# Kernel tuning notes

Measured on AMD Instinct MI355X. Metric: run time of the kernel, lower is better.

## Reference

```python
import jax, jax.numpy as jnp
import numpy as np

B = 16
L = 3600
LATENT = 64
D_MODEL = 128
D_INNER = 256   # expand * d_model
D_STATE = 16
D_CONV = 4
DT_RANK = 8     # ceil(d_model / 16)


def setup_inputs() -> dict:
    key = jax.random.key(0)
    ks = jax.random.split(key, 10)

    def w(k, shape, fan_in):
        return jax.random.normal(k, shape, jnp.float32) / np.float32(np.sqrt(fan_in))

    return {
        "z_sequence": jax.random.normal(ks[0], (B, L, LATENT), jnp.float32),
        # embedding Linear(latent_dim -> mamba_dim)
        "emb_w": w(ks[1], (D_MODEL, LATENT), LATENT),
        "emb_b": jnp.zeros((D_MODEL,), jnp.float32),
        # Mamba in_proj (no bias): d_model -> 2*d_inner
        "in_proj_w": w(ks[2], (2 * D_INNER, D_MODEL), D_MODEL),
        # depthwise causal conv1d (d_inner groups, kernel d_conv) + bias
        "conv_w": w(ks[3], (D_INNER, 1, D_CONV), D_CONV),
        "conv_b": jnp.zeros((D_INNER,), jnp.float32),
        # x_proj (no bias): d_inner -> dt_rank + 2*d_state
        "x_proj_w": w(ks[4], (DT_RANK + 2 * D_STATE, D_INNER), D_INNER),
        # dt_proj: dt_rank -> d_inner, bias init so softplus(b) ~ 0.01
        "dt_proj_w": w(ks[5], (D_INNER, DT_RANK), DT_RANK),
        "dt_proj_b": jnp.full((D_INNER,), np.log(np.expm1(0.01)), jnp.float32),
        # S4D-real init: A = -[1..d_state] per channel
        "A_log": jnp.log(jnp.broadcast_to(
            jnp.arange(1, D_STATE + 1, dtype=jnp.float32), (D_INNER, D_STATE))),
        "D_skip": jnp.ones((D_INNER,), jnp.float32),
        # out_proj (no bias): d_inner -> d_model
        "out_proj_w": w(ks[6], (D_MODEL, D_INNER), D_INNER),
        # LayerNorm(d_model)
        "norm_w": jnp.ones((D_MODEL,), jnp.float32),
        "norm_b": jnp.zeros((D_MODEL,), jnp.float32),
        # classifier Linear(d_model -> 1)
        "cls_w": w(ks[7], (1, D_MODEL), D_MODEL),
        "cls_b": jnp.zeros((1,), jnp.float32),
    }


def _forward(z_sequence, emb_w, emb_b, in_proj_w, conv_w, conv_b, x_proj_w,
             dt_proj_w, dt_proj_b, A_log, D_skip, out_proj_w,
             norm_w, norm_b, cls_w, cls_b):
    silu = jax.nn.silu
    # embedding: (B,L,latent) -> (B,L,d_model)
    x_emb = z_sequence @ emb_w.T + emb_b
    # Mamba in_proj -> x, z  each (B,L,d_inner)
    xz = x_emb @ in_proj_w.T
    x, z = jnp.split(xz, 2, axis=-1)
    # causal depthwise conv over time
    x_ncl = x.transpose(0, 2, 1)  # (B, d_inner, L)
    x_conv = jax.lax.conv_general_dilated(
        x_ncl, conv_w, window_strides=(1,), padding=[(D_CONV - 1, 0)],
        feature_group_count=D_INNER, dimension_numbers=("NCH", "OIH", "NCH"))
    x = silu(x_conv.transpose(0, 2, 1) + conv_b)  # (B,L,d_inner)
    # input-dependent SSM params
    x_dbl = x @ x_proj_w.T  # (B,L,dt_rank+2*d_state)
    dt_in, B_ssm, C_ssm = jnp.split(x_dbl, [DT_RANK, DT_RANK + D_STATE], axis=-1)
    dt = jax.nn.softplus(dt_in @ dt_proj_w.T + dt_proj_b)  # (B,L,d_inner)
    A = -jnp.exp(A_log)  # (d_inner, d_state)

    def step(h, inp):
        x_t, dt_t, B_t, C_t = inp  # (B,d_inner),(B,d_inner),(B,d_state),(B,d_state)
        h = jnp.exp(dt_t[:, :, None] * A) * h + (dt_t * x_t)[:, :, None] * B_t[:, None, :]
        y = jnp.einsum("bds,bs->bd", h, C_t)
        return h, y

    h0 = jnp.zeros((x.shape[0], D_INNER, D_STATE), x.dtype)
    xs = (x.transpose(1, 0, 2), dt.transpose(1, 0, 2),
          B_ssm.transpose(1, 0, 2), C_ssm.transpose(1, 0, 2))
    _, ys = jax.lax.scan(step, h0, xs)  # ys: (L,B,d_inner)
    y = ys.transpose(1, 0, 2) + x * D_skip
    y = y * silu(z)
    out = y @ out_proj_w.T  # (B,L,d_model)
    # take last timestep, LayerNorm, classify
    x_last = out[:, -1, :]
    mu = x_last.mean(-1, keepdims=True)
    var = ((x_last - mu) ** 2).mean(-1, keepdims=True)
    xn = (x_last - mu) / jnp.sqrt(var + 1e-5) * norm_w + norm_b
    logit = xn @ cls_w.T + cls_b  # (B,1)
    return logit.squeeze(-1)      # (B,)


def reference(z_sequence, emb_w, emb_b, in_proj_w, conv_w, conv_b, x_proj_w,
              dt_proj_w, dt_proj_b, A_log, D_skip, out_proj_w,
              norm_w, norm_b, cls_w, cls_b):
    return _forward(z_sequence, emb_w, emb_b, in_proj_w, conv_w, conv_b,
                    x_proj_w, dt_proj_w, dt_proj_b, A_log, D_skip,
                    out_proj_w, norm_w, norm_b, cls_w, cls_b)
```

## Files before the change

kernel.cpp:

```cpp
#include <hip/hip_runtime.h>
#include <hip/hip_bf16.h>
#include <math.h>

#define B_  16
#define L_  3600
#define LAT 64
#define DM  128
#define DI  256
#define DS  16
#define DR  8

#define TT  45
#define NT  80
#define NC  80
#define TC  45
#define THR (-20.0f)

typedef __bf16 v8bf __attribute__((ext_vector_type(8)));
typedef float  v4f  __attribute__((ext_vector_type(4)));
typedef unsigned short v8us __attribute__((ext_vector_type(8)));

#define MFMA16(A, Bf, C) __builtin_amdgcn_mfma_f32_16x16x32_bf16((A), (Bf), (C), 0, 0, 0)

__device__ __forceinline__ float siluf(float v) {
    return v * __builtin_amdgcn_rcpf(1.0f + __expf(-v));
}
__device__ __forceinline__ float softplusf(float v) {
    float r = __logf(1.0f + __expf(v));
    return (v > 15.0f) ? v : r;
}
__device__ __forceinline__ float bf2f(unsigned short u) {
    unsigned int x = ((unsigned int)u) << 16;
    return __builtin_bit_cast(float, x);
}
__device__ __forceinline__ unsigned short f2bf(float f) {
    __hip_bfloat16 h = __float2bfloat16(f);
    return __builtin_bit_cast(unsigned short, h);
}

__global__ __launch_bounds__(64) void k0_combine(
    const float* __restrict__ in_proj_w, const float* __restrict__ emb_w,
    const float* __restrict__ emb_b, const float* __restrict__ x_proj_w,
    float* __restrict__ W1, float* __restrict__ b1,
    unsigned short* __restrict__ W1h, unsigned short* __restrict__ W1l,
    unsigned short* __restrict__ xwh, unsigned short* __restrict__ xwl)
{
    int blk = blockIdx.x, k = threadIdx.x;
    if (blk < DI) {
        int d = blk;
        const float* row = in_proj_w + (size_t)d * DM;
        float acc = 0.f;
        for (int m = 0; m < DM; ++m) acc += row[m] * emb_w[m * LAT + k];
        W1[d * LAT + k] = acc;
        unsigned short h = f2bf(acc);
        W1h[d * LAT + k] = h;
        W1l[d * LAT + k] = f2bf(acc - bf2f(h));
        if (k == 0) {
            float ab = 0.f;
            for (int m = 0; m < DM; ++m) ab += row[m] * emb_b[m];
            b1[d] = ab;
        }
    } else {
        int j = blk - DI;
        int sw = (j & 7) << 3;
        #pragma unroll
        for (int q = 0; q < 4; ++q) {
            int c = k * 4 + q;
            float v = x_proj_w[(size_t)j * DI + c];
            unsigned short h = f2bf(v);
            int idx = j * 256 + (c ^ sw);
            xwh[idx] = h;
            xwl[idx] = f2bf(v - bf2f(h));
        }
    }
}

__global__ __launch_bounds__(256, 3) void k1_front(
    const float* __restrict__ z, const float* __restrict__ conv_w,
    const float* __restrict__ conv_b, const float* __restrict__ dt_proj_w,
    const float* __restrict__ dt_proj_b,
    const unsigned short* __restrict__ W1h, const unsigned short* __restrict__ W1l,
    const unsigned short* __restrict__ xwh, const unsigned short* __restrict__ xwl,
    const float* __restrict__ b1,
    float* __restrict__ Bssm, float* __restrict__ Dcs,
    unsigned int* __restrict__ xd, float* __restrict__ hlast)
{
    __shared__ __align__(16) unsigned char smem[49152];
    __shared__ float dtl[TT][8];
    float* xpre = (float*)smem;
    unsigned short* zth = (unsigned short*)(smem + 32896);
    unsigned short* ztl = (unsigned short*)(smem + 39040);
    unsigned short* xt16 = (unsigned short*)smem;
    unsigned short* xwhL = (unsigned short*)(smem + 24576);
    unsigned short* xwlL = (unsigned short*)(smem + 36864);

    int b = blockIdx.y, tile = blockIdx.x;
    int t0 = tile * TT;
    int t0m3 = t0 - 3;
    int tid = threadIdx.x;
    int lane = tid & 63, wid = tid >> 6;
    int l15 = lane & 15, l4 = lane >> 4;

    if (tile == 0) {
        float4 z4 = make_float4(0.f, 0.f, 0.f, 0.f);
        float4* hl4 = (float4*)(hlast + (size_t)b * (DS * DI));
        #pragma unroll
        for (int i = 0; i < 4; ++i) hl4[tid + i * 256] = z4;
    }

    float4 cw = *(const float4*)(conv_w + tid * 4);
    float cb = conv_b[tid];
    float bias = b1[tid];
    float4 dwA = *(const float4*)(dt_proj_w + (size_t)tid * DR);
    float4 dwB = *(const float4*)(dt_proj_w + (size_t)tid * DR + 4);
    float dbias = dt_proj_b[tid];

    v8bf wh[4][2], wl[4][2];
    {
        int d0w = wid * 64;
        #pragma unroll
        for (int nt = 0; nt < 4; ++nt) {
            int dr = d0w + nt * 16 + l15;
            #pragma unroll
            for (int kb = 0; kb < 2; ++kb) {
                int k0 = kb * 32 + l4 * 8;
                wh[nt][kb] = __builtin_bit_cast(v8bf, *(const v8us*)(W1h + (size_t)dr * LAT + k0));
                wl[nt][kb] = __builtin_bit_cast(v8bf, *(const v8us*)(W1l + (size_t)dr * LAT + k0));
            }
        }
    }

    {
        const float* zb = z + (size_t)b * L_ * LAT;
        for (int i = tid; i < 48 * 8; i += 256) {
            int r = i >> 3, s = i & 7;
            int tg = t0m3 + r;
            float f[8];
            if (tg >= 0) {
                float4 u = *(const float4*)(zb + (size_t)tg * LAT + s * 8);
                float4 v = *(const float4*)(zb + (size_t)tg * LAT + s * 8 + 4);
                f[0]=u.x; f[1]=u.y; f[2]=u.z; f[3]=u.w; f[4]=v.x; f[5]=v.y; f[6]=v.z; f[7]=v.w;
            } else {
                #pragma unroll
                for (int q = 0; q < 8; ++q) f[q] = 0.f;
            }
            v8us hh, ll;
            #pragma unroll
            for (int q = 0; q < 8; ++q) {
                unsigned short h = f2bf(f[q]);
                hh[q] = h;
                ll[q] = f2bf(f[q] - bf2f(h));
            }
            int idx = r * 64 + ((s * 8) ^ ((r & 7) << 3));
            *(v8us*)&zth[idx] = hh;
            *(v8us*)&ztl[idx] = ll;
        }
    }
    __syncthreads();

    int d0w = wid * 64;
    #pragma unroll
    for (int mt = 0; mt < 2; ++mt) {
        int r = mt * 16 + l15;
        int sw = (r & 7) << 3;
        int kb0 = l4 * 8;
        v8bf ah0 = __builtin_bit_cast(v8bf, *(const v8us*)&zth[r * 64 + (kb0 ^ sw)]);
        v8bf ah1 = __builtin_bit_cast(v8bf, *(const v8us*)&zth[r * 64 + ((32 + kb0) ^ sw)]);
        v8bf al0 = __builtin_bit_cast(v8bf, *(const v8us*)&ztl[r * 64 + (kb0 ^ sw)]);
        v8bf al1 = __builtin_bit_cast(v8bf, *(const v8us*)&ztl[r * 64 + ((32 + kb0) ^ sw)]);
        int rr = mt * 16 + l4 * 4;
        #pragma unroll
        for (int nt = 0; nt < 4; ++nt) {
            v4f acc = {0.f, 0.f, 0.f, 0.f};
            acc = MFMA16(ah0, wh[nt][0], acc);
            acc = MFMA16(ah1, wh[nt][1], acc);
            acc = MFMA16(ah0, wl[nt][0], acc);
            acc = MFMA16(ah1, wl[nt][1], acc);
            acc = MFMA16(al0, wh[nt][0], acc);
            acc = MFMA16(al1, wh[nt][1], acc);
            int cc = d0w + nt * 16 + l15;
            xpre[(rr + 0) * 257 + cc] = acc[0];
            xpre[(rr + 1) * 257 + cc] = acc[1];
            xpre[(rr + 2) * 257 + cc] = acc[2];
            xpre[(rr + 3) * 257 + cc] = acc[3];
        }
    }

    v8us xwr[6];
    {
        #pragma unroll
        for (int p = 0; p < 3; ++p) {
            xwr[p]     = *(const v8us*)(xwh + tid * 24 + p * 8);
            xwr[3 + p] = *(const v8us*)(xwl + tid * 24 + p * 8);
        }
    }
    __syncthreads();

    float xr[TT];
    float p0, p1, p2;
    {
        int d = tid;
        p0 = xpre[0 * 257 + d] + ((t0m3 + 0 >= 0) ? bias : 0.f);
        p1 = xpre[1 * 257 + d] + ((t0m3 + 1 >= 0) ? bias : 0.f);
        p2 = xpre[2 * 257 + d] + ((t0m3 + 2 >= 0) ? bias : 0.f);
        #pragma unroll
        for (int r = 3; r < 32; ++r) {
            float cur = xpre[r * 257 + d] + bias;
            float xc = cw.x * p0 + cw.y * p1 + cw.z * p2 + cw.w * cur + cb;
            xr[r - 3] = siluf(xc);
            p0 = p1; p1 = p2; p2 = cur;
        }
    }
    __syncthreads();

    {
        int r = 32 + l15;
        int sw = (r & 7) << 3;
        int kb0 = l4 * 8;
        v8bf ah0 = __builtin_bit_cast(v8bf, *(const v8us*)&zth[r * 64 + (kb0 ^ sw)]);
        v8bf ah1 = __builtin_bit_cast(v8bf, *(const v8us*)&zth[r * 64 + ((32 + kb0) ^ sw)]);
        v8bf al0 = __builtin_bit_cast(v8bf, *(const v8us*)&ztl[r * 64 + (kb0 ^ sw)]);
        v8bf al1 = __builtin_bit_cast(v8bf, *(const v8us*)&ztl[r * 64 + ((32 + kb0) ^ sw)]);
        int rr = l4 * 4;
        #pragma unroll
        for (int nt = 0; nt < 4; ++nt) {
            v4f acc = {0.f, 0.f, 0.f, 0.f};
            acc = MFMA16(ah0, wh[nt][0], acc);
            acc = MFMA16(ah1, wh[nt][1], acc);
            acc = MFMA16(ah0, wl[nt][0], acc);
            acc = MFMA16(ah1, wl[nt][1], acc);
            acc = MFMA16(al0, wh[nt][0], acc);
            acc = MFMA16(al1, wh[nt][1], acc);
            int cc = d0w + nt * 16 + l15;
            xpre[(rr + 0) * 257 + cc] = acc[0];
            xpre[(rr + 1) * 257 + cc] = acc[1];
            xpre[(rr + 2) * 257 + cc] = acc[2];
            xpre[(rr + 3) * 257 + cc] = acc[3];
        }
    }
    __syncthreads();

    {
        int d = tid;
        #pragma unroll
        for (int r = 32; r < 48; ++r) {
            float cur = xpre[(r - 32) * 257 + d] + bias;
            float xc = cw.x * p0 + cw.y * p1 + cw.z * p2 + cw.w * cur + cb;
            xr[r - 3] = siluf(xc);
            p0 = p1; p1 = p2; p2 = cur;
        }
    }
    __syncthreads();

    {
        int d = tid;
        #pragma unroll
        for (int t = 0; t < TT; ++t)
            xt16[t * 256 + (d ^ ((t & 7) << 3))] = f2bf(xr[t]);
        #pragma unroll
        for (int t = TT; t < 48; ++t)
            xt16[t * 256 + (d ^ ((t & 7) << 3))] = 0;
        #pragma unroll
        for (int p = 0; p < 3; ++p) {
            *(v8us*)&xwhL[tid * 24 + p * 8] = xwr[p];
            *(v8us*)&xwlL[tid * 24 + p * 8] = xwr[3 + p];
        }
    }
    __syncthreads();

    if (wid < 3) {
        int mt = wid;
        int rA = mt * 16 + l15;
        int swA = (rA & 7) << 3;
        int jc0 = l15;
        int jc1 = 16 + l15; if (jc1 > 23) jc1 = 23;
        v4f acc0 = {0.f, 0.f, 0.f, 0.f}, acc1 = {0.f, 0.f, 0.f, 0.f};
        #pragma unroll
        for (int kb = 0; kb < 8; ++kb) {
            int k0 = kb * 32 + l4 * 8;
            v8bf xa  = __builtin_bit_cast(v8bf, *(const v8us*)&xt16[rA * 256 + (k0 ^ swA)]);
            int s0 = k0 ^ ((jc0 & 7) << 3);
            int s1 = k0 ^ ((jc1 & 7) << 3);
            v8bf b0h = __builtin_bit_cast(v8bf, *(const v8us*)&xwhL[jc0 * 256 + s0]);
            v8bf b0l = __builtin_bit_cast(v8bf, *(const v8us*)&xwlL[jc0 * 256 + s0]);
            v8bf b1h = __builtin_bit_cast(v8bf, *(const v8us*)&xwhL[jc1 * 256 + s1]);
            v8bf b1l = __builtin_bit_cast(v8bf, *(const v8us*)&xwlL[jc1 * 256 + s1]);
            acc0 = MFMA16(xa, b0h, acc0);
            acc0 = MFMA16(xa, b0l, acc0);
            acc1 = MFMA16(xa, b1h, acc1);
            acc1 = MFMA16(xa, b1l, acc1);
        }
        int rr = mt * 16 + l4 * 4;
        #pragma unroll
        for (int reg = 0; reg < 4; ++reg) {
            int t = rr + reg;
            if (t < TT) {
                size_t tg = (size_t)b * L_ + (t0 + t);
                float v0 = acc0[reg], v1 = acc1[reg];
                if (l15 < 8) {
                    dtl[t][l15] = v0;
                    Bssm[tg * DS + 8 + l15] = v1;
                } else {
                    Bssm[tg * DS + (l15 - 8)] = v0;
                }
            }
        }
    }
    __syncthreads();

    {
        int d = tid;
        unsigned int* xdout = xd + ((size_t)b * L_ + t0) * DI + d;
        float S = 0.f;
        #pragma unroll 5
        for (int t = 0; t < TT; ++t) {
            float4 u = *(const float4*)&dtl[t][0];
            float4 v = *(const float4*)&dtl[t][4];
            float r = dbias + u.x*dwA.x + u.y*dwA.y + u.z*dwA.z + u.w*dwA.w
                            + v.x*dwB.x + v.y*dwB.y + v.z*dwB.z + v.w*dwB.w;
            float dt = softplusf(r);
            unsigned int pack = ((unsigned int)f2bf(dt) << 16) | (unsigned int)f2bf(xr[t]);
            xdout[(size_t)t * DI] = pack;
            S += dt;
        }
        Dcs[((size_t)b * NC + tile) * DI + d] = S;
    }
}

__global__ __launch_bounds__(256) void k3a2_suffix(
    const float* __restrict__ Dcs, float* __restrict__ Rsuf)
{
    int b = blockIdx.x, d = threadIdx.x;
    float R = 0.f;
    for (int c = NC - 1; c >= 0; --c) {
        Rsuf[((size_t)b * NC + c) * DI + d] = R;
        R += Dcs[((size_t)b * NC + c) * DI + d];
    }
}

__global__ __launch_bounds__(512) void k3b_scan(
    const unsigned int* __restrict__ xd,
    const float* __restrict__ Bssm, const float* __restrict__ A_log,
    const float* __restrict__ Rsuf, float* __restrict__ hlast)
{
    int c = blockIdx.x, dg = blockIdx.y, b = blockIdx.z;
    int tid = threadIdx.x;
    int dh = tid & 31;
    int s  = ((tid >> 6) << 1) | ((tid >> 5) & 1);
    int d  = dg * 32 + dh;

    float a = -__expf(A_log[d * DS + s]);
    float R = Rsuf[((size_t)b * NC + c) * DI + d];

    float H = 0.f;
    float S_run = R;
    if (!__all(a * R < THR)) {
        int t0 = c * TC;
        const unsigned int* xp = xd + ((size_t)b * L_ + t0) * DI + d;
        const float* Bp = Bssm + ((size_t)b * L_ + t0) * DS + s;
        {
            unsigned int u4 = xp[(TC-1)*DI];
            float x4 = bf2f((unsigned short)(u4 & 0xffff));
            float d4 = bf2f((unsigned short)(u4 >> 16));
            float B4 = Bp[(TC-1)*DS];
            float e = __expf(a * S_run); H = fmaf(e * d4 * x4, B4, H); S_run += d4;
        }
        for (int j = TC - 5; j >= 0; j -= 4) {
            unsigned int u3 = xp[(j+3)*DI];
            unsigned int u2 = xp[(j+2)*DI];
            unsigned int u1 = xp[(j+1)*DI];
            unsigned int u0 = xp[(j+0)*DI];
            float x3 = bf2f((unsigned short)(u3 & 0xffff)), d3 = bf2f((unsigned short)(u3 >> 16));
            float x2 = bf2f((unsigned short)(u2 & 0xffff)), d2 = bf2f((unsigned short)(u2 >> 16));
            float x1 = bf2f((unsigned short)(u1 & 0xffff)), d1 = bf2f((unsigned short)(u1 >> 16));
            float x0 = bf2f((unsigned short)(u0 & 0xffff)), d0 = bf2f((unsigned short)(u0 >> 16));
            float B3 = Bp[(j+3)*DS];
            float B2 = Bp[(j+2)*DS];
            float B1 = Bp[(j+1)*DS];
            float B0 = Bp[(j+0)*DS];
            float e;
            e = __expf(a * S_run); H = fmaf(e * d3 * x3, B3, H); S_run += d3;
            e = __expf(a * S_run); H = fmaf(e * d2 * x2, B2, H); S_run += d2;
            e = __expf(a * S_run); H = fmaf(e * d1 * x1, B1, H); S_run += d1;
            e = __expf(a * S_run); H = fmaf(e * d0 * x0, B0, H); S_run += d0;
            if (__all(a * S_run < THR)) break;
        }
    }
    if (H != 0.f)
        atomicAdd(hlast + (((size_t)b * DS + s) * DI + d), H);
}

__global__ __launch_bounds__(256) void k4_final(
    const float* __restrict__ z, const float* __restrict__ emb_w,
    const float* __restrict__ emb_b, const float* __restrict__ in_proj_w,
    const float* __restrict__ conv_w, const float* __restrict__ conv_b,
    const float* __restrict__ x_proj_w, const float* __restrict__ D_skip,
    const float* __restrict__ out_proj_w, const float* __restrict__ norm_w,
    const float* __restrict__ norm_b, const float* __restrict__ cls_w,
    const float* __restrict__ cls_b, const float* __restrict__ W1,
    const float* __restrict__ b1, const float* __restrict__ h_last,
    float* __restrict__ out)
{
    __shared__ float zl[4][64];
    __shared__ float xlast[DI];
    __shared__ float xemb[DM];
    __shared__ float Cl[DS];
    __shared__ float ylds[DI];
    __shared__ float olds[DM];
    int b = blockIdx.x, tid = threadIdx.x;
    {
        int r = tid >> 6, k = tid & 63;
        zl[r][k] = z[((size_t)b * L_ + (L_ - 4 + r)) * LAT + k];
    }
    __syncthreads();
    {
        int d = tid;
        const float* wr = W1 + d * LAT;
        float xp[4];
        #pragma unroll
        for (int r = 0; r < 4; ++r) {
            float acc = b1[d];
            for (int k = 0; k < LAT; ++k) acc += zl[r][k] * wr[k];
            xp[r] = acc;
        }
        float4 cwv = *(const float4*)(conv_w + d * 4);
        float xc = cwv.x*xp[0] + cwv.y*xp[1] + cwv.z*xp[2] + cwv.w*xp[3] + conv_b[d];
        xlast[d] = siluf(xc);
    }
    __syncthreads();
    if (tid < DS) {
        float acc = 0.f;
        const float* wr = x_proj_w + (size_t)(DR + DS + tid) * DI;
        for (int k = 0; k < DI; ++k) acc += xlast[k] * wr[k];
        Cl[tid] = acc;
    }
    if (tid >= 64 && tid < 64 + DM) {
        int m = tid - 64;
        float acc = emb_b[m];
        const float* wr = emb_w + (size_t)m * LAT;
        for (int k = 0; k < LAT; ++k) acc += zl[3][k] * wr[k];
        xemb[m] = acc;
    }
    __syncthreads();
    {
        int d = tid;
        float hs = 0.f;
        #pragma unroll
        for (int si = 0; si < DS; ++si)
            hs += h_last[((size_t)b * DS + si) * DI + d] * Cl[si];
        float y = hs + xlast[d] * D_skip[d];
        float zbv = 0.f;
        const float* wr = in_proj_w + (size_t)(DI + d) * DM;
        for (int m = 0; m < DM; ++m) zbv += xemb[m] * wr[m];
        y *= siluf(zbv);
        ylds[d] = y;
    }
    __syncthreads();
    if (tid < DM) {
        float acc = 0.f;
        const float* wr = out_proj_w + (size_t)tid * DI;
        for (int k = 0; k < DI; ++k) acc += ylds[k] * wr[k];
        olds[tid] = acc;
    }
    __syncthreads();
    if (tid < 64) {
        float v0 = olds[tid], v1 = olds[tid + 64];
        float sum = v0 + v1;
        #pragma unroll
        for (int off = 32; off > 0; off >>= 1) sum += __shfl_down(sum, off);
        float mu = __shfl(sum, 0) * (1.0f / 128.0f);
        float dv0 = v0 - mu, dv1 = v1 - mu;
        float vs = dv0 * dv0 + dv1 * dv1;
        #pragma unroll
        for (int off = 32; off > 0; off >>= 1) vs += __shfl_down(vs, off);
        float var = __shfl(vs, 0) * (1.0f / 128.0f);
        float rstd = rsqrtf(var + 1e-5f);
        float xn0 = dv0 * rstd * norm_w[tid] + norm_b[tid];
        float xn1 = dv1 * rstd * norm_w[tid + 64] + norm_b[tid + 64];
        float lg = xn0 * cls_w[tid] + xn1 * cls_w[tid + 64];
        #pragma unroll
        for (int off = 32; off > 0; off >>= 1) lg += __shfl_down(lg, off);
        if (tid == 0) out[b] = lg + cls_b[0];
    }
}

extern "C" void kernel_launch(void* const* d_in, const int* in_sizes, int n_in,
                              void* d_out, int out_size, void* d_ws, size_t ws_size,
                              hipStream_t stream) {
    (void)in_sizes; (void)n_in; (void)out_size;
    const float* z         = (const float*)d_in[0];
    const float* emb_w     = (const float*)d_in[1];
    const float* emb_b     = (const float*)d_in[2];
    const float* in_proj_w = (const float*)d_in[3];
    const float* conv_w    = (const float*)d_in[4];
    const float* conv_b    = (const float*)d_in[5];
    const float* x_proj_w  = (const float*)d_in[6];
    const float* dt_proj_w = (const float*)d_in[7];
    const float* dt_proj_b = (const float*)d_in[8];
    const float* A_log     = (const float*)d_in[9];
    const float* D_skip    = (const float*)d_in[10];
    const float* out_proj_w= (const float*)d_in[11];
    const float* norm_w    = (const float*)d_in[12];
    const float* norm_b    = (const float*)d_in[13];
    const float* cls_w     = (const float*)d_in[14];
    const float* cls_b     = (const float*)d_in[15];
    float* out = (float*)d_out;

    float* ws    = (float*)d_ws;
    float* W1    = ws;
    float* b1    = W1 + 16384;
    float* Bssm  = b1 + 256;
    float* Dcs   = Bssm + 921600;
    float* Rsuf  = Dcs + 327680;
    float* hlast = Rsuf + 327680;
    float* fend  = hlast + 65536;
    unsigned short* W1h  = (unsigned short*)fend;
    unsigned short* W1l  = W1h + 16384;
    unsigned short* xwh  = W1l + 16384;
    unsigned short* xwl  = xwh + 6144;
    unsigned int*   xd   = (unsigned int*)(xwl + 6144);
    size_t needed = ((size_t)(16384 + 256 + 921600 + 327680 + 327680 + 65536)) * 4
                  + ((size_t)(16384 + 16384 + 6144 + 6144)) * 2
                  + (size_t)B_ * L_ * DI * 4;
    if (ws_size < needed) return;

    k0_combine <<<dim3(DI + 24),     dim3(LAT), 0, stream>>>(in_proj_w, emb_w, emb_b, x_proj_w,
                                                             W1, b1, W1h, W1l, xwh, xwl);
    k1_front   <<<dim3(NT, B_),      dim3(256), 0, stream>>>(z, conv_w, conv_b, dt_proj_w, dt_proj_b,
                                                             W1h, W1l, xwh, xwl, b1,
                                                             Bssm, Dcs, xd, hlast);
    k3a2_suffix<<<dim3(B_),          dim3(256), 0, stream>>>(Dcs, Rsuf);
    k3b_scan   <<<dim3(NC, 8, B_),   dim3(512), 0, stream>>>(xd, Bssm, A_log, Rsuf, hlast);
    k4_final   <<<dim3(B_),          dim3(256), 0, stream>>>(z, emb_w, emb_b, in_proj_w, conv_w, conv_b,
                                                             x_proj_w, D_skip, out_proj_w, norm_w, norm_b,
                                                             cls_w, cls_b, W1, b1, hlast, out);
}
```

Measured before the change: 116.1 us.

## Shrink k1 LDS footprint, raise occupancy, read x_proj weights from global

The front kernel now computes the input projection in three 16-row chunks that reuse a smaller xpre buffer, which cuts shared memory from 48KB to about 28KB and raises the launch-bounds occupancy target from 3 to 5 blocks. The x_proj weight fragments are read straight from global/L2 instead of being staged in LDS. The suffix-sum kernel is unrolled to batch 40 loads ahead of the dependent adds and stores. Together these aim to overlap more latency through higher occupancy and memory-level parallelism, at the cost of an extra barrier per chunk, possible register pressure under the tighter bound, and global-latency MFMA operand loads.

```diff
diff --git a/kernel.cpp b/kernel.cpp
--- a/kernel.cpp
+++ b/kernel.cpp
@@ -75,7 +75,7 @@
     }
 }
 
-__global__ __launch_bounds__(256, 3) void k1_front(
+__global__ __launch_bounds__(256, 5) void k1_front(
     const float* __restrict__ z, const float* __restrict__ conv_w,
     const float* __restrict__ conv_b, const float* __restrict__ dt_proj_w,
     const float* __restrict__ dt_proj_b,
@@ -85,14 +85,12 @@
     float* __restrict__ Bssm, float* __restrict__ Dcs,
     unsigned int* __restrict__ xd, float* __restrict__ hlast)
 {
-    __shared__ __align__(16) unsigned char smem[49152];
+    __shared__ __align__(16) unsigned char smem[28736];
     __shared__ float dtl[TT][8];
     float* xpre = (float*)smem;
-    unsigned short* zth = (unsigned short*)(smem + 32896);
-    unsigned short* ztl = (unsigned short*)(smem + 39040);
+    unsigned short* zth = (unsigned short*)(smem + 16448);
+    unsigned short* ztl = (unsigned short*)(smem + 22592);
     unsigned short* xt16 = (unsigned short*)smem;
-    unsigned short* xwhL = (unsigned short*)(smem + 24576);
-    unsigned short* xwlL = (unsigned short*)(smem + 36864);
 
     int b = blockIdx.y, tile = blockIdx.x;
     int t0 = tile * TT;
@@ -116,8 +114,8 @@
     float dbias = dt_proj_b[tid];
 
     v8bf wh[4][2], wl[4][2];
-    {
-        int d0w = wid * 64;
+    int d0w = wid * 64;
+    {
         #pragma unroll
         for (int nt = 0; nt < 4; ++nt) {
             int dr = d0w + nt * 16 + l15;
@@ -158,99 +156,63 @@
     }
     __syncthreads();
 
-    int d0w = wid * 64;
+    float xr[TT];
+    float p0 = 0.f, p1 = 0.f, p2 = 0.f;
+
     #pragma unroll
-    for (int mt = 0; mt < 2; ++mt) {
-        int r = mt * 16 + l15;
-        int sw = (r & 7) << 3;
-        int kb0 = l4 * 8;
-        v8bf ah0 = __builtin_bit_cast(v8bf, *(const v8us*)&zth[r * 64 + (kb0 ^ sw)]);
-        v8bf ah1 = __builtin_bit_cast(v8bf, *(const v8us*)&zth[r * 64 + ((32 + kb0) ^ sw)]);
-        v8bf al0 = __builtin_bit_cast(v8bf, *(const v8us*)&ztl[r * 64 + (kb0 ^ sw)]);
-        v8bf al1 = __builtin_bit_cast(v8bf, *(const v8us*)&ztl[r * 64 + ((32 + kb0) ^ sw)]);
-        int rr = mt * 16 + l4 * 4;
-        #pragma unroll
-        for (int nt = 0; nt < 4; ++nt) {
-            v4f acc = {0.f, 0.f, 0.f, 0.f};
-            acc = MFMA16(ah0, wh[nt][0], acc);
-            acc = MFMA16(ah1, wh[nt][1], acc);
-            acc = MFMA16(ah0, wl[nt][0], acc);
-            acc = MFMA16(ah1, wl[nt][1], acc);
-            acc = MFMA16(al0, wh[nt][0], acc);
-            acc = MFMA16(al1, wh[nt][1], acc);
-            int cc = d0w + nt * 16 + l15;
-            xpre[(rr + 0) * 257 + cc] = acc[0];
-            xpre[(rr + 1) * 257 + cc] = acc[1];
-            xpre[(rr + 2) * 257 + cc] = acc[2];
-            xpre[(rr + 3) * 257 + cc] = acc[3];
-        }
-    }
-
-    v8us xwr[6];
-    {
-        #pragma unroll
-        for (int p = 0; p < 3; ++p) {
-            xwr[p]     = *(const v8us*)(xwh + tid * 24 + p * 8);
-            xwr[3 + p] = *(const v8us*)(xwl + tid * 24 + p * 8);
-        }
-    }
-    __syncthreads();
-
-    float xr[TT];
-    float p0, p1, p2;
-    {
-        int d = tid;
-        p0 = xpre[0 * 257 + d] + ((t0m3 + 0 >= 0) ? bias : 0.f);
-        p1 = xpre[1 * 257 + d] + ((t0m3 + 1 >= 0) ? bias : 0.f);
-        p2 = xpre[2 * 257 + d] + ((t0m3 + 2 >= 0) ? bias : 0.f);
-        #pragma unroll
-        for (int r = 3; r < 32; ++r) {
-            float cur = xpre[r * 257 + d] + bias;
-            float xc = cw.x * p0 + cw.y * p1 + cw.z * p2 + cw.w * cur + cb;
-            xr[r - 3] = siluf(xc);
-            p0 = p1; p1 = p2; p2 = cur;
-        }
-    }
-    __syncthreads();
-
-    {
-        int r = 32 + l15;
-        int sw = (r & 7) << 3;
-        int kb0 = l4 * 8;
-        v8bf ah0 = __builtin_bit_cast(v8bf, *(const v8us*)&zth[r * 64 + (kb0 ^ sw)]);
-        v8bf ah1 = __builtin_bit_cast(v8bf, *(const v8us*)&zth[r * 64 + ((32 + kb0) ^ sw)]);
-        v8bf al0 = __builtin_bit_cast(v8bf, *(const v8us*)&ztl[r * 64 + (kb0 ^ sw)]);
-        v8bf al1 = __builtin_bit_cast(v8bf, *(const v8us*)&ztl[r * 64 + ((32 + kb0) ^ sw)]);
-        int rr = l4 * 4;
-        #pragma unroll
-        for (int nt = 0; nt < 4; ++nt) {
-            v4f acc = {0.f, 0.f, 0.f, 0.f};
-            acc = MFMA16(ah0, wh[nt][0], acc);
-            acc = MFMA16(ah1, wh[nt][1], acc);
-            acc = MFMA16(ah0, wl[nt][0], acc);
-            acc = MFMA16(ah1, wl[nt][1], acc);
-            acc = MFMA16(al0, wh[nt][0], acc);
-            acc = MFMA16(al1, wh[nt][1], acc);
-            int cc = d0w + nt * 16 + l15;
-            xpre[(rr + 0) * 257 + cc] = acc[0];
-            xpre[(rr + 1) * 257 + cc] = acc[1];
-            xpre[(rr + 2) * 257 + cc] = acc[2];
-            xpre[(rr + 3) * 257 + cc] = acc[3];
-        }
-    }
-    __syncthreads();
-
-    {
-        int d = tid;
-        #pragma unroll
-        for (int r = 32; r < 48; ++r) {
-            float cur = xpre[(r - 32) * 257 + d] + bias;
-            float xc = cw.x * p0 + cw.y * p1 + cw.z * p2 + cw.w * cur + cb;
-            xr[r - 3] = siluf(xc);
-            p0 = p1; p1 = p2; p2 = cur;
-        }
-    }
-    __syncthreads();
+    for (int mt = 0; mt < 3; ++mt) {
+        {
+            int r = mt * 16 + l15;
+            int sw = (r & 7) << 3;
+            int kb0 = l4 * 8;
+            v8bf ah0 = __builtin_bit_cast(v8bf, *(const v8us*)&zth[r * 64 + (kb0 ^ sw)]);
+            v8bf ah1 = __builtin_bit_cast(v8bf, *(const v8us*)&zth[r * 64 + ((32 + kb0) ^ sw)]);
+            v8bf al0 = __builtin_bit_cast(v8bf, *(const v8us*)&ztl[r * 64 + (kb0 ^ sw)]);
+            v8bf al1 = __builtin_bit_cast(v8bf, *(const v8us*)&ztl[r * 64 + ((32 + kb0) ^ sw)]);
+            int rr = l4 * 4;
+            #pragma unroll
+            for (int nt = 0; nt < 4; ++nt) {
+                v4f acc = {0.f, 0.f, 0.f, 0.f};
+                acc = MFMA16(ah0, wh[nt][0], acc);
+                acc = MFMA16(ah1, wh[nt][1], acc);
+                acc = MFMA16(ah0, wl[nt][0], acc);
+                acc = MFMA16(ah1, wl[nt][1], acc);
+                acc = MFMA16(al0, wh[nt][0], acc);
+                acc = MFMA16(al1, wh[nt][1], acc);
+                int cc = d0w + nt * 16 + l15;
+                xpre[(rr + 0) * 257 + cc] = acc[0];
+                xpre[(rr + 1) * 257 + cc] = acc[1];
+                xpre[(rr + 2) * 257 + cc] = acc[2];
+                xpre[(rr + 3) * 257 + cc] = acc[3];
+            }
+        }
+        __syncthreads();
+        {
+            int d = tid;
+            if (mt == 0) {
+                p0 = xpre[0 * 257 + d] + ((t0m3 + 0 >= 0) ? bias : 0.f);
+                p1 = xpre[1 * 257 + d] + ((t0m3 + 1 >= 0) ? bias : 0.f);
+                p2 = xpre[2 * 257 + d] + ((t0m3 + 2 >= 0) ? bias : 0.f);
+                #pragma unroll
+                for (int r = 3; r < 16; ++r) {
+                    float cur = xpre[r * 257 + d] + bias;
+                    float xc = cw.x * p0 + cw.y * p1 + cw.z * p2 + cw.w * cur + cb;
+                    xr[r - 3] = siluf(xc);
+                    p0 = p1; p1 = p2; p2 = cur;
+                }
+            } else {
+                int rbase = mt * 16;
+                #pragma unroll
+                for (int q = 0; q < 16; ++q) {
+                    float cur = xpre[q * 257 + d] + bias;
+                    float xc = cw.x * p0 + cw.y * p1 + cw.z * p2 + cw.w * cur + cb;
+                    xr[rbase + q - 3] = siluf(xc);
+                    p0 = p1; p1 = p2; p2 = cur;
+                }
+            }
+        }
+        __syncthreads();
+    }
 
     {
         int d = tid;
@@ -260,11 +222,6 @@
         #pragma unroll
         for (int t = TT; t < 48; ++t)
             xt16[t * 256 + (d ^ ((t & 7) << 3))] = 0;
-        #pragma unroll
-        for (int p = 0; p < 3; ++p) {
-            *(v8us*)&xwhL[tid * 24 + p * 8] = xwr[p];
-            *(v8us*)&xwlL[tid * 24 + p * 8] = xwr[3 + p];
-        }
     }
     __syncthreads();
 
@@ -281,10 +238,10 @@
             v8bf xa  = __builtin_bit_cast(v8bf, *(const v8us*)&xt16[rA * 256 + (k0 ^ swA)]);
             int s0 = k0 ^ ((jc0 & 7) << 3);
             int s1 = k0 ^ ((jc1 & 7) << 3);
-            v8bf b0h = __builtin_bit_cast(v8bf, *(const v8us*)&xwhL[jc0 * 256 + s0]);
-            v8bf b0l = __builtin_bit_cast(v8bf, *(const v8us*)&xwlL[jc0 * 256 + s0]);
-            v8bf b1h = __builtin_bit_cast(v8bf, *(const v8us*)&xwhL[jc1 * 256 + s1]);
-            v8bf b1l = __builtin_bit_cast(v8bf, *(const v8us*)&xwlL[jc1 * 256 + s1]);
+            v8bf b0h = __builtin_bit_cast(v8bf, *(const v8us*)(xwh + jc0 * 256 + s0));
+            v8bf b0l = __builtin_bit_cast(v8bf, *(const v8us*)(xwl + jc0 * 256 + s0));
+            v8bf b1h = __builtin_bit_cast(v8bf, *(const v8us*)(xwh + jc1 * 256 + s1));
+            v8bf b1l = __builtin_bit_cast(v8bf, *(const v8us*)(xwl + jc1 * 256 + s1));
             acc0 = MFMA16(xa, b0h, acc0);
             acc0 = MFMA16(xa, b0l, acc0);
             acc1 = MFMA16(xa, b1h, acc1);
@@ -331,11 +288,18 @@
     const float* __restrict__ Dcs, float* __restrict__ Rsuf)
 {
     int b = blockIdx.x, d = threadIdx.x;
+    const float* src = Dcs + (size_t)b * NC * DI + d;
+    float* dst = Rsuf + (size_t)b * NC * DI + d;
+    float v[40];
     float R = 0.f;
-    for (int c = NC - 1; c >= 0; --c) {
-        Rsuf[((size_t)b * NC + c) * DI + d] = R;
-        R += Dcs[((size_t)b * NC + c) * DI + d];
-    }
+    #pragma unroll
+    for (int i = 0; i < 40; ++i) v[i] = src[(size_t)(NC - 1 - i) * DI];
+    #pragma unroll
+    for (int i = 0; i < 40; ++i) { dst[(size_t)(NC - 1 - i) * DI] = R; R += v[i]; }
+    #pragma unroll
+    for (int i = 0; i < 40; ++i) v[i] = src[(size_t)(39 - i) * DI];
+    #pragma unroll
+    for (int i = 0; i < 40; ++i) { dst[(size_t)(39 - i) * DI] = R; R += v[i]; }
 }
 
 __global__ __launch_bounds__(512) void k3b_scan(
```

After: 176.5 us. 1.52x slower.
